# Performance work log

Hardware: AMD Instinct MI355X
Metric: run time of the kernel (lower is better)

## Reference

```python
import jax, jax.numpy as jnp
import numpy as np

B, S, E, C = 256, 1024, 256, 4  # batch, seq_len, embed_dim, output_dim
NB = 4  # number of branches (sorted keys: acc, bvp, eda, temp)


def setup_inputs() -> dict:
    key = jax.random.key(0)
    ks = jax.random.split(key, 6)
    return {
        "x_acc": jax.random.normal(ks[0], (B, S, E), dtype=jnp.float32),
        "x_bvp": jax.random.normal(ks[1], (B, S, E), dtype=jnp.float32),
        "x_eda": jax.random.normal(ks[2], (B, S, E), dtype=jnp.float32),
        "x_temp": jax.random.normal(ks[3], (B, S, E), dtype=jnp.float32),
        "W": jax.random.normal(ks[4], (C, E), dtype=jnp.float32) * 0.05,
        "b": jax.random.normal(ks[5], (C,), dtype=jnp.float32) * 0.05,
    }


def reference(x_acc, x_bvp, x_eda, x_temp, W, b):
    # Branches processed in sorted key order: acc, bvp, eda, temp.
    branches = jnp.stack([x_acc, x_bvp, x_eda, x_temp], axis=1)  # [B, NB, S, E]
    # permute + AdaptiveAvgPool1d(1) + squeeze == mean over the seq dim
    pooled = branches.mean(axis=2)  # [B, NB, E]
    # shared Linear(E, C); dropout is identity in eval mode
    logits = jax.nn.relu(jnp.einsum("bne,ce->bnc", pooled, W) + b)  # [B, NB, C]
    probs = jax.nn.softmax(logits, axis=-1)  # [B, NB, C]
    # Hard voting: argmax per branch, vote fraction per class.
    preds = jnp.argmax(probs, axis=-1)  # [B, NB] int
    votes = jax.nn.one_hot(preds, C, dtype=jnp.float32)  # [B, NB, C]
    final_probabilities = votes.mean(axis=1)  # [B, C], counts / len(branch_keys)
    return final_probabilities
```

## Files before the change

kernel.cpp:

```cpp
#include <hip/hip_runtime.h>

#define BB 256
#define SS 1024
#define EE 256
#define CC 4

__global__ __launch_bounds__(512) void pool_vote_kernel(
    const float* __restrict__ x0, const float* __restrict__ x1,
    const float* __restrict__ x2, const float* __restrict__ x3,
    const float* __restrict__ W, const float* __restrict__ bias,
    float* __restrict__ out)
{
    const int bn = blockIdx.x;
    const int b  = bn >> 2;
    const int n  = bn & 3;
    const float* __restrict__ x =
        (n == 0) ? x0 : (n == 1) ? x1 : (n == 2) ? x2 : x3;

    const int tid = threadIdx.x;
    const int e4  = tid & 63;
    const int sl  = tid >> 6;

    const size_t base = (size_t)b * ((size_t)SS * EE)
                      + (size_t)sl * EE
                      + (size_t)(e4 << 2);
    const float4* __restrict__ p = (const float4*)(x + base);
    const size_t step = (size_t)8 * (EE / 4);

    float4 a0 = make_float4(0.f, 0.f, 0.f, 0.f);
    float4 a1 = make_float4(0.f, 0.f, 0.f, 0.f);
    float4 a2 = make_float4(0.f, 0.f, 0.f, 0.f);
    float4 a3 = make_float4(0.f, 0.f, 0.f, 0.f);
    #pragma unroll 2
    for (int i = 0; i < SS / 8; i += 4) {
        float4 v0 = p[(size_t)(i + 0) * step];
        float4 v1 = p[(size_t)(i + 1) * step];
        float4 v2 = p[(size_t)(i + 2) * step];
        float4 v3 = p[(size_t)(i + 3) * step];
        a0.x += v0.x; a0.y += v0.y; a0.z += v0.z; a0.w += v0.w;
        a1.x += v1.x; a1.y += v1.y; a1.z += v1.z; a1.w += v1.w;
        a2.x += v2.x; a2.y += v2.y; a2.z += v2.z; a2.w += v2.w;
        a3.x += v3.x; a3.y += v3.y; a3.z += v3.z; a3.w += v3.w;
    }
    float4 acc;
    acc.x = (a0.x + a1.x) + (a2.x + a3.x);
    acc.y = (a0.y + a1.y) + (a2.y + a3.y);
    acc.z = (a0.z + a1.z) + (a2.z + a3.z);
    acc.w = (a0.w + a1.w) + (a2.w + a3.w);

    __shared__ float4 red[512];
    red[tid] = acc;
    __syncthreads();

    if (tid < 64) {
        const float inv = 1.0f / (float)SS;
        float4 s0 = red[tid];
        float4 s1 = red[tid + 64];
        float4 s2 = red[tid + 128];
        float4 s3 = red[tid + 192];
        float4 s4 = red[tid + 256];
        float4 s5 = red[tid + 320];
        float4 s6 = red[tid + 384];
        float4 s7 = red[tid + 448];
        float4 pool;
        pool.x = ((s0.x + s1.x) + (s2.x + s3.x)) + ((s4.x + s5.x) + (s6.x + s7.x));
        pool.y = ((s0.y + s1.y) + (s2.y + s3.y)) + ((s4.y + s5.y) + (s6.y + s7.y));
        pool.z = ((s0.z + s1.z) + (s2.z + s3.z)) + ((s4.z + s5.z) + (s6.z + s7.z));
        pool.w = ((s0.w + s1.w) + (s2.w + s3.w)) + ((s4.w + s5.w) + (s6.w + s7.w));
        pool.x *= inv; pool.y *= inv; pool.z *= inv; pool.w *= inv;

        const float4* __restrict__ W4 = (const float4*)W;
        float d0, d1, d2, d3;
        {
            float4 w0 = W4[0 * 64 + tid];
            float4 w1 = W4[1 * 64 + tid];
            float4 w2 = W4[2 * 64 + tid];
            float4 w3 = W4[3 * 64 + tid];
            d0 = pool.x * w0.x + pool.y * w0.y + pool.z * w0.z + pool.w * w0.w;
            d1 = pool.x * w1.x + pool.y * w1.y + pool.z * w1.z + pool.w * w1.w;
            d2 = pool.x * w2.x + pool.y * w2.y + pool.z * w2.z + pool.w * w2.w;
            d3 = pool.x * w3.x + pool.y * w3.y + pool.z * w3.z + pool.w * w3.w;
        }
        #pragma unroll
        for (int off = 32; off >= 1; off >>= 1) {
            d0 += __shfl_down(d0, off, 64);
            d1 += __shfl_down(d1, off, 64);
            d2 += __shfl_down(d2, off, 64);
            d3 += __shfl_down(d3, off, 64);
        }

        if (tid == 0) {
            float l0 = fmaxf(d0 + bias[0], 0.f);
            float l1 = fmaxf(d1 + bias[1], 0.f);
            float l2 = fmaxf(d2 + bias[2], 0.f);
            float l3 = fmaxf(d3 + bias[3], 0.f);
            int pred = 0; float best = l0;
            if (l1 > best) { best = l1; pred = 1; }
            if (l2 > best) { best = l2; pred = 2; }
            if (l3 > best) { best = l3; pred = 3; }
            atomicAdd(&out[b * CC + pred], 0.25f);
        }
    }
}

extern "C" void kernel_launch(void* const* d_in, const int* in_sizes, int n_in,
                              void* d_out, int out_size, void* d_ws, size_t ws_size,
                              hipStream_t stream) {
    const float* x_acc  = (const float*)d_in[0];
    const float* x_bvp  = (const float*)d_in[1];
    const float* x_eda  = (const float*)d_in[2];
    const float* x_temp = (const float*)d_in[3];
    const float* W      = (const float*)d_in[4];
    const float* bias   = (const float*)d_in[5];
    float* out = (float*)d_out;

    hipMemsetAsync(out, 0, (size_t)out_size * sizeof(float), stream);

    pool_vote_kernel<<<dim3(BB * 4), dim3(512), 0, stream>>>(
        x_acc, x_bvp, x_eda, x_temp, W, bias, out);
}
```

Baseline: 780.3 us.

## Split sequence pooling across segment blocks with a separate combine-and-vote kernel

Splits the mean-pooling over the sequence into 8 segments per (batch, branch), so 8192 smaller blocks write partial sums to workspace. A second small kernel combines the partials, applies the linear layer, ReLU and argmax, and atomically adds the votes. The aim is more blocks and more memory requests in flight for this bandwidth-bound reduction, at the cost of an extra launch and workspace traffic. The old fused kernel stays as a fallback when the workspace is too small, with its unroll changed.

```diff
diff --git a/kernel.cpp b/kernel.cpp
--- a/kernel.cpp
+++ b/kernel.cpp
@@ -4,6 +4,115 @@
 #define SS 1024
 #define EE 256
 #define CC 4
+
+#define SEGS 8
+#define SEGROWS (SS / SEGS)
+#define NBLK1 (BB * 4 * SEGS)
+
+__global__ __launch_bounds__(256) void pool_partial_kernel(
+    const float* __restrict__ x0, const float* __restrict__ x1,
+    const float* __restrict__ x2, const float* __restrict__ x3,
+    float* __restrict__ ws)
+{
+    const int g   = blockIdx.x;
+    const int bn  = g >> 3;
+    const int seg = g & (SEGS - 1);
+    const int b   = bn >> 2;
+    const int n   = bn & 3;
+    const float* __restrict__ x =
+        (n == 0) ? x0 : (n == 1) ? x1 : (n == 2) ? x2 : x3;
+
+    const int tid = threadIdx.x;
+    const int e4  = tid & 63;
+    const int sl  = tid >> 6;
+
+    const size_t base = (size_t)b * ((size_t)SS * EE)
+                      + (size_t)(seg * SEGROWS + sl) * EE
+                      + (size_t)(e4 << 2);
+    const float4* __restrict__ p = (const float4*)(x + base);
+    const size_t step = (size_t)4 * (EE / 4);
+
+    float4 a0 = make_float4(0.f, 0.f, 0.f, 0.f);
+    float4 a1 = make_float4(0.f, 0.f, 0.f, 0.f);
+    #pragma unroll 4
+    for (int i = 0; i < SEGROWS / 4; i += 2) {
+        float4 v0 = p[(size_t)i * step];
+        float4 v1 = p[(size_t)(i + 1) * step];
+        a0.x += v0.x; a0.y += v0.y; a0.z += v0.z; a0.w += v0.w;
+        a1.x += v1.x; a1.y += v1.y; a1.z += v1.z; a1.w += v1.w;
+    }
+    float4 acc;
+    acc.x = a0.x + a1.x; acc.y = a0.y + a1.y;
+    acc.z = a0.z + a1.z; acc.w = a0.w + a1.w;
+
+    __shared__ float4 red[256];
+    red[tid] = acc;
+    __syncthreads();
+
+    if (tid < 64) {
+        float4 s0 = red[tid];
+        float4 s1 = red[tid + 64];
+        float4 s2 = red[tid + 128];
+        float4 s3 = red[tid + 192];
+        float4 part;
+        part.x = (s0.x + s1.x) + (s2.x + s3.x);
+        part.y = (s0.y + s1.y) + (s2.y + s3.y);
+        part.z = (s0.z + s1.z) + (s2.z + s3.z);
+        part.w = (s0.w + s1.w) + (s2.w + s3.w);
+        ((float4*)ws)[(size_t)g * 64 + tid] = part;
+    }
+}
+
+__global__ __launch_bounds__(64) void combine_vote_kernel(
+    const float* __restrict__ ws, const float* __restrict__ W,
+    const float* __restrict__ bias, float* __restrict__ out)
+{
+    const int bn  = blockIdx.x;
+    const int b   = bn >> 2;
+    const int tid = threadIdx.x;
+
+    const float4* __restrict__ ws4 = (const float4*)ws;
+    float4 pool = make_float4(0.f, 0.f, 0.f, 0.f);
+    #pragma unroll
+    for (int seg = 0; seg < SEGS; ++seg) {
+        float4 v = ws4[(size_t)(bn * SEGS + seg) * 64 + tid];
+        pool.x += v.x; pool.y += v.y; pool.z += v.z; pool.w += v.w;
+    }
+    const float inv = 1.0f / (float)SS;
+    pool.x *= inv; pool.y *= inv; pool.z *= inv; pool.w *= inv;
+
+    const float4* __restrict__ W4 = (const float4*)W;
+    float d0, d1, d2, d3;
+    {
+        float4 w0 = W4[0 * 64 + tid];
+        float4 w1 = W4[1 * 64 + tid];
+        float4 w2 = W4[2 * 64 + tid];
+        float4 w3 = W4[3 * 64 + tid];
+        d0 = pool.x * w0.x + pool.y * w0.y + pool.z * w0.z + pool.w * w0.w;
+        d1 = pool.x * w1.x + pool.y * w1.y + pool.z * w1.z + pool.w * w1.w;
+        d2 = pool.x * w2.x + pool.y * w2.y + pool.z * w2.z + pool.w * w2.w;
+        d3 = pool.x * w3.x + pool.y * w3.y + pool.z * w3.z + pool.w * w3.w;
+    }
+    #pragma unroll
+    for (int off = 32; off >= 1; off >>= 1) {
+        d0 += __shfl_down(d0, off, 64);
+        d1 += __shfl_down(d1, off, 64);
+        d2 += __shfl_down(d2, off, 64);
+        d3 += __shfl_down(d3, off, 64);
+    }
+
+    if (tid == 0) {
+        float l0 = fmaxf(d0 + bias[0], 0.f);
+        float l1 = fmaxf(d1 + bias[1], 0.f);
+        float l2 = fmaxf(d2 + bias[2], 0.f);
+        float l3 = fmaxf(d3 + bias[3], 0.f);
+        int pred = 0; float best = l0;
+        if (l1 > best) { best = l1; pred = 1; }
+        if (l2 > best) { best = l2; pred = 2; }
+        if (l3 > best) { best = l3; pred = 3; }
+        atomicAdd(&out[b * CC + pred], 0.25f);
+    }
+}
 
 __global__ __launch_bounds__(512) void pool_vote_kernel(
     const float* __restrict__ x0, const float* __restrict__ x1,
@@ -29,24 +138,16 @@
 
     float4 a0 = make_float4(0.f, 0.f, 0.f, 0.f);
     float4 a1 = make_float4(0.f, 0.f, 0.f, 0.f);
-    float4 a2 = make_float4(0.f, 0.f, 0.f, 0.f);
-    float4 a3 = make_float4(0.f, 0.f, 0.f, 0.f);
-    #pragma unroll 2
-    for (int i = 0; i < SS / 8; i += 4) {
-        float4 v0 = p[(size_t)(i + 0) * step];
+    #pragma unroll 4
+    for (int i = 0; i < SS / 8; i += 2) {
+        float4 v0 = p[(size_t)i * step];
         float4 v1 = p[(size_t)(i + 1) * step];
-        float4 v2 = p[(size_t)(i + 2) * step];
-        float4 v3 = p[(size_t)(i + 3) * step];
         a0.x += v0.x; a0.y += v0.y; a0.z += v0.z; a0.w += v0.w;
         a1.x += v1.x; a1.y += v1.y; a1.z += v1.z; a1.w += v1.w;
-        a2.x += v2.x; a2.y += v2.y; a2.z += v2.z; a2.w += v2.w;
-        a3.x += v3.x; a3.y += v3.y; a3.z += v3.z; a3.w += v3.w;
     }
     float4 acc;
-    acc.x = (a0.x + a1.x) + (a2.x + a3.x);
-    acc.y = (a0.y + a1.y) + (a2.y + a3.y);
-    acc.z = (a0.z + a1.z) + (a2.z + a3.z);
-    acc.w = (a0.w + a1.w) + (a2.w + a3.w);
+    acc.x = a0.x + a1.x; acc.y = a0.y + a1.y;
+    acc.z = a0.z + a1.z; acc.w = a0.w + a1.w;
 
     __shared__ float4 red[512];
     red[tid] = acc;
@@ -116,6 +217,15 @@
 
     hipMemsetAsync(out, 0, (size_t)out_size * sizeof(float), stream);
 
-    pool_vote_kernel<<<dim3(BB * 4), dim3(512), 0, stream>>>(
-        x_acc, x_bvp, x_eda, x_temp, W, bias, out);
-}
+    const size_t ws_need = (size_t)NBLK1 * 64 * sizeof(float4);
+    if (d_ws != nullptr && ws_size >= ws_need) {
+        float* ws = (float*)d_ws;
+        pool_partial_kernel<<<dim3(NBLK1), dim3(256), 0, stream>>>(
+            x_acc, x_bvp, x_eda, x_temp, ws);
+        combine_vote_kernel<<<dim3(BB * 4), dim3(64), 0, stream>>>(
+            ws, W, bias, out);
+    } else {
+        pool_vote_kernel<<<dim3(BB * 4), dim3(512), 0, stream>>>(
+            x_acc, x_bvp, x_eda, x_temp, W, bias, out);
+    }
+}
```

Result: slower. 801.0 us (+2.6%).
